# Performance work log

Hardware: AMD Instinct MI355X
Metric: run time of the kernel (lower is better)

The kernel has to match this reference:

```python
import jax, jax.numpy as jnp
import numpy as np

NUM_HEADS = 16
NUM_KV_HEADS = 4
HEAD_DIM = 128
ROPE_BASE = 10000.0


def _rotate_half(x):
    half = x.shape[-1] // 2
    return jnp.concatenate([-x[..., half:], x[..., :half]], axis=-1)


def _rope_cos_sin(seq_len, dim, dtype):
    inv_freq = 1.0 / (ROPE_BASE ** (jnp.arange(0, dim, 2, dtype=jnp.float32) / dim))
    t = jnp.arange(seq_len, dtype=jnp.float32)
    freqs = jnp.outer(t, inv_freq)            # (T, dim/2)
    emb = jnp.concatenate([freqs, freqs], -1)  # (T, dim)
    return jnp.cos(emb).astype(dtype), jnp.sin(emb).astype(dtype)


def setup_inputs() -> dict:
    key = jax.random.key(0)
    ks = jax.random.split(key, 5)
    B, T, D = 2, 2048, 2048
    Dkv = NUM_KV_HEADS * HEAD_DIM
    s = 1.0 / np.sqrt(D)
    return {
        "x": jax.random.normal(ks[0], (B, T, D), jnp.float32),
        "Wq": jax.random.normal(ks[1], (D, D), jnp.float32) * s,
        "Wk": jax.random.normal(ks[2], (D, Dkv), jnp.float32) * s,
        "Wv": jax.random.normal(ks[3], (D, Dkv), jnp.float32) * s,
        "Wo": jax.random.normal(ks[4], (D, D), jnp.float32) * s,
    }


def reference(x, Wq, Wk, Wv, Wo):
    B, T, D = x.shape
    H, Hkv, hd = NUM_HEADS, NUM_KV_HEADS, HEAD_DIM
    # projections, split heads -> (B, H, T, hd)
    q = (x @ Wq).reshape(B, T, H, hd).transpose(0, 2, 1, 3)
    k = (x @ Wk).reshape(B, T, Hkv, hd).transpose(0, 2, 1, 3)
    v = (x @ Wv).reshape(B, T, Hkv, hd).transpose(0, 2, 1, 3)
    # RoPE on q and k
    cos, sin = _rope_cos_sin(T, hd, x.dtype)  # (T, hd) each
    q = q * cos + _rotate_half(q) * sin
    k = k * cos + _rotate_half(k) * sin
    # GQA: repeat_interleave KV heads to match Q heads
    r = H // Hkv
    k = jnp.repeat(k, r, axis=1)
    v = jnp.repeat(v, r, axis=1)
    # causal SDPA
    scale = hd ** -0.5
    scores = jnp.einsum('bhqd,bhkd->bhqk', q, k) * scale
    causal = jnp.tril(jnp.ones((T, T), bool))
    scores = jnp.where(causal, scores, jnp.finfo(scores.dtype).min)
    attn = jax.nn.softmax(scores, axis=-1)
    out = jnp.einsum('bhqk,bhkd->bhqd', attn, v)
    out = out.transpose(0, 2, 1, 3).reshape(B, T, D)
    return out @ Wo
```

## Files before the change

### kernel.cpp

```cpp
#include <hip/hip_runtime.h>

typedef __bf16 bf16x8 __attribute__((ext_vector_type(8)));
typedef float floatx4 __attribute__((ext_vector_type(4)));
typedef unsigned short ushort_t;
typedef ushort_t ushortx4 __attribute__((ext_vector_type(4)));
typedef float floatx4v __attribute__((ext_vector_type(4)));

typedef __attribute__((address_space(1))) void gvoid;
typedef __attribute__((address_space(3))) void svoid;

#define MFMA16(a, b, c) __builtin_amdgcn_mfma_f32_16x16x32_bf16(a, b, c, 0, 0, 0)

__device__ __forceinline__ ushort_t f2bf(float f) {
  unsigned u = __builtin_bit_cast(unsigned, f);
  u += 0x7fffu + ((u >> 16) & 1u);
  return (ushort_t)(u >> 16);
}

__device__ __forceinline__ void gld16(const ushort_t* g, ushort_t* l) {
  __builtin_amdgcn_global_load_lds((gvoid*)(g), (svoid*)(l), 16, 0, 0);
}

__global__ __launch_bounds__(256) void k_prep(const floatx4v* __restrict__ xin,
                                              ushortx4* __restrict__ x_bf,
                                              const float* __restrict__ Wq,
                                              const float* __restrict__ Wk,
                                              const float* __restrict__ Wv,
                                              const float* __restrict__ Wo,
                                              ushort_t* __restrict__ WqkvT,
                                              ushort_t* __restrict__ WoT) {
  __shared__ float tile[64][65];
  if (blockIdx.x < 8192) {
    int i = blockIdx.x * 256 + threadIdx.x;
    floatx4v v = xin[i];
    ushortx4 o;
    o[0] = f2bf(v[0]); o[1] = f2bf(v[1]); o[2] = f2bf(v[2]); o[3] = f2bf(v[3]);
    x_bf[i] = o;
    return;
  }
  const int pb = blockIdx.x - 8192;
  const int byy = pb / 80;
  const int bx = pb - byy * 80;
  const float* in;
  ushort_t* out;
  int N, cx;
  if (bx < 32)      { in = Wq; out = WqkvT;              N = 2048; cx = bx; }
  else if (bx < 40) { in = Wk; out = WqkvT + 2048*2048;  N = 512;  cx = bx - 32; }
  else if (bx < 48) { in = Wv; out = WqkvT + 2560*2048;  N = 512;  cx = bx - 40; }
  else              { in = Wo; out = WoT;                N = 2048; cx = bx - 48; }
  const int c0 = cx * 64;
  const int k0 = byy * 64;
  const int tx = threadIdx.x & 63;
  const int ty = threadIdx.x >> 6;
#pragma unroll
  for (int i = 0; i < 16; i++) {
    int row = i * 4 + ty;
    tile[tx][row] = in[(k0 + row) * N + c0 + tx];
  }
  __syncthreads();
#pragma unroll
  for (int i = 0; i < 16; i++) {
    int nr = i * 4 + ty;
    out[(c0 + nr) * 2048 + k0 + tx] = f2bf(tile[nr][tx]);
  }
}

__global__ __launch_bounds__(512, 2) void k_gemm_qkv(const ushort_t* __restrict__ A,
                                                     const ushort_t* __restrict__ Bt,
                                                     ushort_t* __restrict__ Qh,
                                                     ushort_t* __restrict__ Kh,
                                                     ushort_t* __restrict__ Vt) {
  __shared__ __align__(16) ushort_t smem[65536];

  const int tid = threadIdx.x;
  const int lane = tid & 63;
  const int w = tid >> 6;
  const int wm = w >> 2;
  const int wn = w & 3;
  const int r = lane & 15;
  const int q = lane >> 4;
  const int rx7 = r & 7;

  const int bid = blockIdx.x;
  const int s = bid >> 3;
  const int mhi = (s >= 12) ? 1 : 0;
  const int n_t = s - mhi * 12;
  const int m_t = (bid & 7) * 2 + mhi;
  const int m0 = m_t * 256;
  const int n0 = n_t * 256;

  const int srow = tid >> 3;
  const int sch = tid & 7;
  const int scol = (sch ^ (srow & 7)) * 8;
  const ushort_t* Ag = A + (m0 + srow) * 2048 + scol;
  const ushort_t* Bg = Bt + (n0 + srow) * 2048 + scol;

#define STG_A(bufc, half, kk) do {                                                        \
    gld16(Ag + ((half) * 128) * 2048 + (kk),                                              \
          smem + (bufc) * 16384 + ((half) * 128 + srow) * 64 + sch * 8);                  \
    gld16(Ag + ((half) * 128 + 64) * 2048 + (kk),                                         \
          smem + (bufc) * 16384 + ((half) * 128 + 64 + srow) * 64 + sch * 8);             \
  } while (0)
#define STG_B(bufc, half, kk) do {                                                        \
    gld16(Bg + ((half) * 128) * 2048 + (kk),                                              \
          smem + 32768 + (bufc) * 16384 + ((half) * 128 + srow) * 64 + sch * 8);          \
    gld16(Bg + ((half) * 128 + 64) * 2048 + (kk),                                         \
          smem + 32768 + (bufc) * 16384 + ((half) * 128 + 64 + srow) * 64 + sch * 8);     \
  } while (0)

  const int arow = wm * 16 + r;
  const int brow = wn * 16 + r;
  const int ch0 = (q ^ rx7) * 8;
  const int ch1 = ((4 + q) ^ rx7) * 8;

  const floatx4 fz = {0.f, 0.f, 0.f, 0.f};
  floatx4 acc[8][4];
#pragma unroll
  for (int i = 0; i < 8; i++)
#pragma unroll
    for (int j = 0; j < 4; j++) acc[i][j] = fz;

  STG_A(0, 0, 0); STG_B(0, 0, 0); STG_B(0, 1, 0); STG_A(0, 1, 0);

  for (int t = 0; t < 32; ++t) {
    const int c = t & 1;
    const int nc = 1 - c;
    const ushort_t* Ac = smem + c * 16384;
    const ushort_t* Bc = smem + 32768 + c * 16384;
    const bool st = (t + 1 < 32);
    const int kt1 = (t + 1) * 64;

    bf16x8 a0f[4][2], a1f[4][2], b0f[2][2], b1f[2][2];

    asm volatile("s_waitcnt vmcnt(4)" ::: "memory");
    asm volatile("s_barrier" ::: "memory");
#pragma unroll
    for (int mf = 0; mf < 4; mf++) {
      const ushort_t* ap = Ac + (mf * 32 + arow) * 64;
      a0f[mf][0] = *(const bf16x8*)(ap + ch0);
      a0f[mf][1] = *(const bf16x8*)(ap + ch1);
    }
#pragma unroll
    for (int nq = 0; nq < 2; nq++) {
      const ushort_t* bp = Bc + (nq * 64 + brow) * 64;
      b0f[nq][0] = *(const bf16x8*)(bp + ch0);
      b0f[nq][1] = *(const bf16x8*)(bp + ch1);
    }
    if (st) STG_A(nc, 0, kt1);
    __builtin_amdgcn_s_setprio(1);
#pragma unroll
    for (int ks = 0; ks < 2; ks++)
#pragma unroll
      for (int mf = 0; mf < 4; mf++)
#pragma unroll
        for (int nq = 0; nq < 2; nq++)
          acc[mf][nq] = MFMA16(a0f[mf][ks], b0f[nq][ks], acc[mf][nq]);
    __builtin_amdgcn_s_setprio(0);

    if (st) { asm volatile("s_waitcnt vmcnt(4)" ::: "memory"); }
    else    { asm volatile("s_waitcnt vmcnt(2)" ::: "memory"); }
    asm volatile("s_barrier" ::: "memory");
#pragma unroll
    for (int nq = 0; nq < 2; nq++) {
      const ushort_t* bp = Bc + (128 + nq * 64 + brow) * 64;
      b1f[nq][0] = *(const bf16x8*)(bp + ch0);
      b1f[nq][1] = *(const bf16x8*)(bp + ch1);
    }
    if (st) STG_B(nc, 0, kt1);
    __builtin_amdgcn_s_setprio(1);
#pragma unroll
    for (int ks = 0; ks < 2; ks++)
#pragma unroll
      for (int mf = 0; mf < 4; mf++)
#pragma unroll
        for (int nq = 0; nq < 2; nq++)
          acc[mf][2 + nq] = MFMA16(a0f[mf][ks], b1f[nq][ks], acc[mf][2 + nq]);
    __builtin_amdgcn_s_setprio(0);

    if (st) { asm volatile("s_waitcnt vmcnt(4)" ::: "memory"); }
    else    { asm volatile("s_waitcnt vmcnt(0)" ::: "memory"); }
    asm volatile("s_barrier" ::: "memory");
#pragma unroll
    for (int mf = 0; mf < 4; mf++) {
      const ushort_t* ap = Ac + (128 + mf * 32 + arow) * 64;
      a1f[mf][0] = *(const bf16x8*)(ap + ch0);
      a1f[mf][1] = *(const bf16x8*)(ap + ch1);
    }
    if (st) STG_B(nc, 1, kt1);
    __builtin_amdgcn_s_setprio(1);
#pragma unroll
    for (int ks = 0; ks < 2; ks++)
#pragma unroll
      for (int mf = 0; mf < 4; mf++)
#pragma unroll
        for (int nq = 0; nq < 2; nq++)
          acc[4 + mf][2 + nq] = MFMA16(a1f[mf][ks], b1f[nq][ks], acc[4 + mf][2 + nq]);
    __builtin_amdgcn_s_setprio(0);

    if (st) STG_A(nc, 1, kt1);
    __builtin_amdgcn_s_setprio(1);
#pragma unroll
    for (int ks = 0; ks < 2; ks++)
#pragma unroll
      for (int mf = 0; mf < 4; mf++)
#pragma unroll
        for (int nq = 0; nq < 2; nq++)
          acc[4 + mf][nq] = MFMA16(a1f[mf][ks], b0f[nq][ks], acc[4 + mf][nq]);
    __builtin_amdgcn_s_setprio(0);
  }
#undef STG_A
#undef STG_B

  const int bb = m0 >> 11;
  const int tbase = (m0 & 2047) + wm * 16;

  if (n0 < 2048) {
    const float scale = 0.08838834764831845f;
    const int d = wn * 16 + r;
    const float invf = __expf(-0.14391156643f * (float)d);
#pragma unroll
    for (int pr = 0; pr < 2; pr++) {
      ushort_t* dst = Qh + ((bb * 16 + (n0 >> 7) + pr) * 2048) * 128;
#pragma unroll
      for (int mf = 0; mf < 8; mf++)
#pragma unroll
        for (int reg = 0; reg < 4; reg++) {
          const int tt = tbase + mf * 32 + q * 4 + reg;
          float sn, cs;
          __sincosf((float)tt * invf, &sn, &cs);
          const float lo = acc[mf][2 * pr][reg];
          const float hi = acc[mf][2 * pr + 1][reg];
          dst[tt * 128 + d] = f2bf((lo * cs - hi * sn) * scale);
          dst[tt * 128 + d + 64] = f2bf((hi * cs + lo * sn) * scale);
        }
    }
  } else if (n0 < 2560) {
    const int d = wn * 16 + r;
    const float invf = __expf(-0.14391156643f * (float)d);
#pragma unroll
    for (int pr = 0; pr < 2; pr++) {
      ushort_t* dst = Kh + ((bb * 4 + ((n0 - 2048) >> 7) + pr) * 2048) * 128;
#pragma unroll
      for (int mf = 0; mf < 8; mf++)
#pragma unroll
        for (int reg = 0; reg < 4; reg++) {
          const int tt = tbase + mf * 32 + q * 4 + reg;
          float sn, cs;
          __sincosf((float)tt * invf, &sn, &cs);
          const float lo = acc[mf][2 * pr][reg];
          const float hi = acc[mf][2 * pr + 1][reg];
          dst[tt * 128 + d] = f2bf(lo * cs - hi * sn);
          dst[tt * 128 + d + 64] = f2bf(hi * cs + lo * sn);
        }
    }
  } else {
#pragma unroll
    for (int pr = 0; pr < 2; pr++) {
      ushort_t* dst = Vt + ((bb * 4 + ((n0 - 2560) >> 7) + pr) * 128) * 2048;
#pragma unroll
      for (int nq = 0; nq < 2; nq++) {
        const int d = nq * 64 + wn * 16 + r;
#pragma unroll
        for (int mf = 0; mf < 8; mf++) {
          const int t0 = tbase + mf * 32 + q * 4;
          ushortx4 pk;
#pragma unroll
          for (int reg = 0; reg < 4; reg++) pk[reg] = f2bf(acc[mf][2 * pr + nq][reg]);
          *(ushortx4*)(dst + d * 2048 + t0) = pk;
        }
      }
    }
  }
}

__global__ __launch_bounds__(256) void k_flash(const ushort_t* __restrict__ Qh,
                                               const ushort_t* __restrict__ Kh,
                                               const ushort_t* __restrict__ Vt,
                                               ushort_t* __restrict__ attn) {
  __shared__ __align__(16) ushort_t smem[36864];

  const int t = threadIdx.x;
  const int w = t >> 6;
  const int lane = t & 63;
  const int r = lane & 15;
  const int q = lane >> 4;
  const int rx = r & 7;

  const int xcd = blockIdx.x & 7;
  const int s_ = blockIdx.x >> 3;
  const int bh2 = s_ & 3;
  const int st = s_ >> 2;
  const int ti = 31 - st;
  const int bh = xcd * 4 + bh2;
  const int jmax = ti + 1;

  const int b = bh >> 4;
  const int h = bh & 15;
  const int hkv = h >> 2;

  const ushort_t* Qg = Qh + (bh * 2048) * 128;
  const ushort_t* Kg = Kh + ((b * 4 + hkv) * 2048) * 128;
  const ushort_t* Vg = Vt + ((b * 4 + hkv) * 128) * 2048;
  ushort_t* Pw = smem + 32768 + w * 1024;

  {
    const int qrow = t >> 4;
    const int gcq = (t & 15) ^ (qrow & 7);
#pragma unroll
    for (int i = 0; i < 4; i++)
      gld16(Qg + (ti * 64 + i * 16 + qrow) * 128 + gcq * 8, smem + i * 2048 + t * 8);
  }
  __syncthreads();
  bf16x8 aq[4];
#pragma unroll
  for (int ks = 0; ks < 4; ks++) {
    const int pp = ((ks * 4 + q) ^ rx) * 8;
    aq[ks] = *(const bf16x8*)(smem + (w * 16 + r) * 128 + pp);
  }
  __syncthreads();

  const int krow = t >> 4;
  const int gck = (t & 15) ^ (krow & 7);
  const int vrow = t >> 3;
  const int gcv = (t & 7) ^ (vrow & 7);

#pragma unroll
  for (int i = 0; i < 4; i++)
    gld16(Kg + (i * 16 + krow) * 128 + gck * 8, smem + i * 2048 + t * 8);
#pragma unroll
  for (int i = 0; i < 4; i++)
    gld16(Vg + (i * 32 + vrow) * 2048 + gcv * 8, smem + 16384 + i * 2048 + t * 8);

  const floatx4 fz = {0.f, 0.f, 0.f, 0.f};
  floatx4 acc[8];
#pragma unroll
  for (int nd = 0; nd < 8; nd++) acc[nd] = fz;
  float lsum[4];
#pragma unroll
  for (int reg = 0; reg < 4; reg++) lsum[reg] = 0.f;

  for (int j = 0; j < jmax; j++) {
    const int c = j & 1;
    const ushort_t* Kc = smem + c * 8192;
    const ushort_t* Vc = smem + 16384 + c * 8192;
    __syncthreads();
    if (j + 1 < jmax) {
      ushort_t* Kn = smem + (1 - c) * 8192;
      ushort_t* Vn = smem + 16384 + (1 - c) * 8192;
#pragma unroll
      for (int i = 0; i < 4; i++)
        gld16(Kg + ((j + 1) * 64 + i * 16 + krow) * 128 + gck * 8, Kn + i * 2048 + t * 8);
#pragma unroll
      for (int i = 0; i < 4; i++)
        gld16(Vg + (i * 32 + vrow) * 2048 + (j + 1) * 64 + gcv * 8, Vn + i * 2048 + t * 8);
    }

    floatx4 s[4];
#pragma unroll
    for (int ni = 0; ni < 4; ni++) s[ni] = fz;
#pragma unroll
    for (int ks = 0; ks < 4; ks++) {
      const int pp = ((ks * 4 + q) ^ rx) * 8;
#pragma unroll
      for (int ni = 0; ni < 4; ni++) {
        bf16x8 bk = *(const bf16x8*)(Kc + (ni * 16 + r) * 128 + pp);
        s[ni] = MFMA16(aq[ks], bk, s[ni]);
      }
    }
    if (j == jmax - 1) {
#pragma unroll
      for (int ni = 0; ni < 4; ni++)
#pragma unroll
        for (int reg = 0; reg < 4; reg++) {
          const int row_l = w * 16 + q * 4 + reg;
          const int col_l = ni * 16 + r;
          if (col_l > row_l) s[ni][reg] = -1e30f;
        }
    }
#pragma unroll
    for (int ni = 0; ni < 4; ni++)
#pragma unroll
      for (int reg = 0; reg < 4; reg++)
        s[ni][reg] = __expf(s[ni][reg] - 8.0f);
#pragma unroll
    for (int reg = 0; reg < 4; reg++)
      lsum[reg] += (s[0][reg] + s[1][reg]) + (s[2][reg] + s[3][reg]);
#pragma unroll
    for (int ni = 0; ni < 4; ni++)
#pragma unroll
      for (int reg = 0; reg < 4; reg++) {
        const int lr = q * 4 + reg;
        const int col = ni * 16 + r;
        Pw[lr * 64 + ((col >> 3) ^ (lr & 7)) * 8 + (col & 7)] = f2bf(s[ni][reg]);
      }
#pragma unroll
    for (int ks = 0; ks < 2; ks++) {
      const int pp = ((ks * 4 + q) ^ rx) * 8;
      bf16x8 ap = *(const bf16x8*)(Pw + r * 64 + pp);
#pragma unroll
      for (int nd = 0; nd < 8; nd++) {
        bf16x8 bv = *(const bf16x8*)(Vc + (nd * 16 + r) * 64 + pp);
        acc[nd] = MFMA16(ap, bv, acc[nd]);
      }
    }
  }

#pragma unroll
  for (int reg = 0; reg < 4; reg++) {
#pragma unroll
    for (int d = 1; d < 16; d <<= 1)
      lsum[reg] += __shfl_xor(lsum[reg], d);
  }
  ushort_t* dst = attn + (b * 2048 + ti * 64) * 2048 + h * 128;
#pragma unroll
  for (int reg = 0; reg < 4; reg++) {
    const int row_l = w * 16 + q * 4 + reg;
    const float inv = 1.0f / lsum[reg];
#pragma unroll
    for (int nd = 0; nd < 8; nd++)
      dst[row_l * 2048 + nd * 16 + r] = f2bf(acc[nd][reg] * inv);
  }
}

__global__ __launch_bounds__(256) void k_gemm_out(const ushort_t* __restrict__ A,
                                                  const ushort_t* __restrict__ Bt,
                                                  float* __restrict__ out) {
  __shared__ __align__(16) ushort_t As[2][4096];
  __shared__ __align__(16) ushort_t Bs[2][4096];
  const int t = threadIdx.x;
  const int w = t >> 6;
  const int lane = t & 63;
  const int r = lane & 15;
  const int q = lane >> 4;
  const int m0 = blockIdx.y * 128;
  const int n0 = blockIdx.x * 128;

  const int srow = t >> 2;
  const int gc = (t & 3) ^ ((t >> 3) & 3);
  const int a_g0 = (m0 + srow) * 2048 + gc * 8;
  const int b_g0 = (n0 + srow) * 2048 + gc * 8;

  const int pos8 = (q ^ ((r >> 1) & 3)) * 8;
  const int a_off = (w * 32 + r) * 32 + pos8;
  const int b_off = r * 32 + pos8;

  const floatx4 fz = {0.f, 0.f, 0.f, 0.f};
  floatx4 acc[2][8];
#pragma unroll
  for (int i = 0; i < 2; i++)
#pragma unroll
    for (int jj = 0; jj < 8; jj++) acc[i][jj] = fz;

  gld16(A + a_g0, As[0] + t * 8);
  gld16(A + a_g0 + 64 * 2048, As[0] + 2048 + t * 8);
  gld16(Bt + b_g0, Bs[0] + t * 8);
  gld16(Bt + b_g0 + 64 * 2048, Bs[0] + 2048 + t * 8);

  for (int it = 0; it < 64; it++) {
    const int c = it & 1;
    __syncthreads();
    if (it < 63) {
      const int kt = (it + 1) * 32;
      gld16(A + a_g0 + kt, As[1 - c] + t * 8);
      gld16(A + a_g0 + 64 * 2048 + kt, As[1 - c] + 2048 + t * 8);
      gld16(Bt + b_g0 + kt, Bs[1 - c] + t * 8);
      gld16(Bt + b_g0 + 64 * 2048 + kt, Bs[1 - c] + 2048 + t * 8);
    }
    bf16x8 af0 = *(const bf16x8*)(As[c] + a_off);
    bf16x8 af1 = *(const bf16x8*)(As[c] + a_off + 512);
    bf16x8 bfv[8];
#pragma unroll
    for (int ni = 0; ni < 8; ni++) bfv[ni] = *(const bf16x8*)(Bs[c] + b_off + ni * 512);
#pragma unroll
    for (int ni = 0; ni < 8; ni++) {
      acc[0][ni] = MFMA16(af0, bfv[ni], acc[0][ni]);
      acc[1][ni] = MFMA16(af1, bfv[ni], acc[1][ni]);
    }
  }

#pragma unroll
  for (int mi = 0; mi < 2; mi++)
#pragma unroll
    for (int ni = 0; ni < 8; ni++)
#pragma unroll
      for (int reg = 0; reg < 4; reg++)
        out[(m0 + w * 32 + mi * 16 + q * 4 + reg) * 2048 + n0 + ni * 16 + r] =
            acc[mi][ni][reg];
}

extern "C" void kernel_launch(void* const* d_in, const int* in_sizes, int n_in,
                              void* d_out, int out_size, void* d_ws, size_t ws_size,
                              hipStream_t stream) {
  (void)in_sizes; (void)n_in; (void)out_size; (void)ws_size;
  const float* x  = (const float*)d_in[0];
  const float* Wq = (const float*)d_in[1];
  const float* Wk = (const float*)d_in[2];
  const float* Wv = (const float*)d_in[3];
  const float* Wo = (const float*)d_in[4];
  float* out = (float*)d_out;

  char* ws = (char*)d_ws;
  ushort_t* x_bf   = (ushort_t*)(ws);
  ushort_t* WqkvT  = (ushort_t*)(ws + 16777216);
  ushort_t* WoT    = (ushort_t*)(ws + 29360128);
  ushort_t* Qh     = (ushort_t*)(ws + 37748736);
  ushort_t* Kh     = (ushort_t*)(ws + 54525952);
  ushort_t* Vt     = (ushort_t*)(ws + 58720256);
  ushort_t* attn   = (ushort_t*)(ws + 62914560);

  k_prep<<<8192 + 2560, 256, 0, stream>>>((const floatx4v*)x, (ushortx4*)x_bf,
                                          Wq, Wk, Wv, Wo, WqkvT, WoT);
  k_gemm_qkv<<<192, 512, 0, stream>>>(x_bf, WqkvT, Qh, Kh, Vt);
  k_flash<<<1024, 256, 0, stream>>>(Qh, Kh, Vt, attn);
  k_gemm_out<<<dim3(16, 32), 256, 0, stream>>>(attn, WoT, out);
}
```

Baseline: 280.6 us.

## Rewrite output projection GEMM with 256x128 tiles, BK=64 and split-phase pipelining

```diff
diff --git a/kernel.cpp b/kernel.cpp
--- a/kernel.cpp
+++ b/kernel.cpp
@@ -422,70 +422,126 @@
   }
 }
 
-__global__ __launch_bounds__(256) void k_gemm_out(const ushort_t* __restrict__ A,
-                                                  const ushort_t* __restrict__ Bt,
-                                                  float* __restrict__ out) {
-  __shared__ __align__(16) ushort_t As[2][4096];
-  __shared__ __align__(16) ushort_t Bs[2][4096];
-  const int t = threadIdx.x;
-  const int w = t >> 6;
-  const int lane = t & 63;
+__global__ __launch_bounds__(512, 2) void k_gemm_out(const ushort_t* __restrict__ A,
+                                                     const ushort_t* __restrict__ Bt,
+                                                     float* __restrict__ out) {
+  __shared__ __align__(16) ushort_t smem[49152];
+
+  const int tid = threadIdx.x;
+  const int lane = tid & 63;
+  const int w = tid >> 6;
+  const int wm = w >> 2;
+  const int wn = w & 3;
   const int r = lane & 15;
   const int q = lane >> 4;
-  const int m0 = blockIdx.y * 128;
-  const int n0 = blockIdx.x * 128;
-
-  const int srow = t >> 2;
-  const int gc = (t & 3) ^ ((t >> 3) & 3);
-  const int a_g0 = (m0 + srow) * 2048 + gc * 8;
-  const int b_g0 = (n0 + srow) * 2048 + gc * 8;
-
-  const int pos8 = (q ^ ((r >> 1) & 3)) * 8;
-  const int a_off = (w * 32 + r) * 32 + pos8;
-  const int b_off = r * 32 + pos8;
+  const int rx7 = r & 7;
+
+  const int bid = blockIdx.x;
+  const int s = bid >> 3;
+  const int m_t = (bid & 7) * 2 + (s >> 4);
+  const int n_t = s & 15;
+  const int m0 = m_t * 256;
+  const int n0 = n_t * 128;
+
+  const int srow = tid >> 3;
+  const int sch = tid & 7;
+  const int scol = (sch ^ (srow & 7)) * 8;
+  const ushort_t* Ag = A + (m0 + srow) * 2048 + scol;
+  const ushort_t* Bg = Bt + (n0 + srow) * 2048 + scol;
+
+#define STG_A(bufc, half, kk) do {                                                        \
+    gld16(Ag + ((half) * 128) * 2048 + (kk),                                              \
+          smem + (bufc) * 16384 + ((half) * 128 + srow) * 64 + sch * 8);                  \
+    gld16(Ag + ((half) * 128 + 64) * 2048 + (kk),                                         \
+          smem + (bufc) * 16384 + ((half) * 128 + 64 + srow) * 64 + sch * 8);             \
+  } while (0)
+#define STG_B(bufc, kk) do {                                                              \
+    gld16(Bg + (kk),                                                                      \
+          smem + 32768 + (bufc) * 8192 + srow * 64 + sch * 8);                            \
+    gld16(Bg + 64 * 2048 + (kk),                                                          \
+          smem + 32768 + (bufc) * 8192 + (64 + srow) * 64 + sch * 8);                     \
+  } while (0)
+
+  const int arow = wm * 16 + r;
+  const int brow = wn * 16 + r;
+  const int ch0 = (q ^ rx7) * 8;
+  const int ch1 = ((4 + q) ^ rx7) * 8;
 
   const floatx4 fz = {0.f, 0.f, 0.f, 0.f};
-  floatx4 acc[2][8];
-#pragma unroll
-  for (int i = 0; i < 2; i++)
-#pragma unroll
-    for (int jj = 0; jj < 8; jj++) acc[i][jj] = fz;
-
-  gld16(A + a_g0, As[0] + t * 8);
-  gld16(A + a_g0 + 64 * 2048, As[0] + 2048 + t * 8);
-  gld16(Bt + b_g0, Bs[0] + t * 8);
-  gld16(Bt + b_g0 + 64 * 2048, Bs[0] + 2048 + t * 8);
-
-  for (int it = 0; it < 64; it++) {
-    const int c = it & 1;
-    __syncthreads();
-    if (it < 63) {
-      const int kt = (it + 1) * 32;
-      gld16(A + a_g0 + kt, As[1 - c] + t * 8);
-      gld16(A + a_g0 + 64 * 2048 + kt, As[1 - c] + 2048 + t * 8);
-      gld16(Bt + b_g0 + kt, Bs[1 - c] + t * 8);
-      gld16(Bt + b_g0 + 64 * 2048 + kt, Bs[1 - c] + 2048 + t * 8);
-    }
-    bf16x8 af0 = *(const bf16x8*)(As[c] + a_off);
-    bf16x8 af1 = *(const bf16x8*)(As[c] + a_off + 512);
-    bf16x8 bfv[8];
-#pragma unroll
-    for (int ni = 0; ni < 8; ni++) bfv[ni] = *(const bf16x8*)(Bs[c] + b_off + ni * 512);
-#pragma unroll
-    for (int ni = 0; ni < 8; ni++) {
-      acc[0][ni] = MFMA16(af0, bfv[ni], acc[0][ni]);
-      acc[1][ni] = MFMA16(af1, bfv[ni], acc[1][ni]);
-    }
-  }
-
-#pragma unroll
-  for (int mi = 0; mi < 2; mi++)
-#pragma unroll
-    for (int ni = 0; ni < 8; ni++)
+  floatx4 acc[8][2];
+#pragma unroll
+  for (int i = 0; i < 8; i++)
+#pragma unroll
+    for (int j = 0; j < 2; j++) acc[i][j] = fz;
+
+  STG_A(0, 0, 0); STG_B(0, 0); STG_A(0, 1, 0);
+
+  for (int t = 0; t < 32; ++t) {
+    const int c = t & 1;
+    const int nc = 1 - c;
+    const ushort_t* Ac = smem + c * 16384;
+    const ushort_t* Bc = smem + 32768 + c * 8192;
+    const bool st = (t + 1 < 32);
+    const int kt1 = (t + 1) * 64;
+
+    bf16x8 a0f[4][2], a1f[4][2], bf[2][2];
+
+    asm volatile("s_waitcnt vmcnt(2)" ::: "memory");
+    asm volatile("s_barrier" ::: "memory");
+#pragma unroll
+    for (int mf = 0; mf < 4; mf++) {
+      const ushort_t* ap = Ac + (mf * 32 + arow) * 64;
+      a0f[mf][0] = *(const bf16x8*)(ap + ch0);
+      a0f[mf][1] = *(const bf16x8*)(ap + ch1);
+    }
+#pragma unroll
+    for (int nq = 0; nq < 2; nq++) {
+      const ushort_t* bp = Bc + (nq * 64 + brow) * 64;
+      bf[nq][0] = *(const bf16x8*)(bp + ch0);
+      bf[nq][1] = *(const bf16x8*)(bp + ch1);
+    }
+    if (st) STG_A(nc, 0, kt1);
+    __builtin_amdgcn_s_setprio(1);
+#pragma unroll
+    for (int ks = 0; ks < 2; ks++)
+#pragma unroll
+      for (int mf = 0; mf < 4; mf++)
+#pragma unroll
+        for (int nq = 0; nq < 2; nq++)
+          acc[mf][nq] = MFMA16(a0f[mf][ks], bf[nq][ks], acc[mf][nq]);
+    __builtin_amdgcn_s_setprio(0);
+
+    if (st) { asm volatile("s_waitcnt vmcnt(2)" ::: "memory"); }
+    else    { asm volatile("s_waitcnt vmcnt(0)" ::: "memory"); }
+    asm volatile("s_barrier" ::: "memory");
+#pragma unroll
+    for (int mf = 0; mf < 4; mf++) {
+      const ushort_t* ap = Ac + (128 + mf * 32 + arow) * 64;
+      a1f[mf][0] = *(const bf16x8*)(ap + ch0);
+      a1f[mf][1] = *(const bf16x8*)(ap + ch1);
+    }
+    if (st) { STG_B(nc, kt1); STG_A(nc, 1, kt1); }
+    __builtin_amdgcn_s_setprio(1);
+#pragma unroll
+    for (int ks = 0; ks < 2; ks++)
+#pragma unroll
+      for (int mf = 0; mf < 4; mf++)
+#pragma unroll
+        for (int nq = 0; nq < 2; nq++)
+          acc[4 + mf][nq] = MFMA16(a1f[mf][ks], bf[nq][ks], acc[4 + mf][nq]);
+    __builtin_amdgcn_s_setprio(0);
+  }
+#undef STG_A
+#undef STG_B
+
+#pragma unroll
+  for (int mf = 0; mf < 8; mf++)
+#pragma unroll
+    for (int nq = 0; nq < 2; nq++)
 #pragma unroll
       for (int reg = 0; reg < 4; reg++)
-        out[(m0 + w * 32 + mi * 16 + q * 4 + reg) * 2048 + n0 + ni * 16 + r] =
-            acc[mi][ni][reg];
+        out[(m0 + mf * 32 + wm * 16 + q * 4 + reg) * 2048 + n0 + nq * 64 + wn * 16 + r] =
+            acc[mf][nq][reg];
 }
 
 extern "C" void kernel_launch(void* const* d_in, const int* in_sizes, int n_in,
@@ -512,5 +568,5 @@
                                           Wq, Wk, Wv, Wo, WqkvT, WoT);
   k_gemm_qkv<<<192, 512, 0, stream>>>(x_bf, WqkvT, Qh, Kh, Vt);
   k_flash<<<1024, 256, 0, stream>>>(Qh, Kh, Vt, attn);
-  k_gemm_out<<<dim3(16, 32), 256, 0, stream>>>(attn, WoT, out);
-}
+  k_gemm_out<<<256, 512, 0, stream>>>(attn, WoT, out);
+}
```

Result: faster. 263.3 us (median of 2 runs) (-6.2%).
